# Optimization experiments

Measured on AMD Instinct MI355X. Metric: run time of the kernel, lower is better.

Reference implementation:

```python
import jax, jax.numpy as jnp
import numpy as np

NUM_HEADS = 12
D = 768
HD = D // NUM_HEADS  # 64

def setup_inputs() -> dict:
    key = jax.random.key(0)
    ks = jax.random.split(key, 9)
    s = 0.02
    return {
        "x": jax.random.normal(ks[0], (4, 2048, D), dtype=jnp.float32),
        "QW_w": jax.random.normal(ks[1], (D, D), dtype=jnp.float32) * s,
        "QW_b": jax.random.normal(ks[2], (D,), dtype=jnp.float32) * s,
        "KW_w": jax.random.normal(ks[3], (D, D), dtype=jnp.float32) * s,
        "KW_b": jax.random.normal(ks[4], (D,), dtype=jnp.float32) * s,
        "VW_w": jax.random.normal(ks[5], (D, D), dtype=jnp.float32) * s,
        "VW_b": jax.random.normal(ks[6], (D,), dtype=jnp.float32) * s,
        "OW_w": jax.random.normal(ks[7], (D, D), dtype=jnp.float32) * s,
        "OW_b": jax.random.normal(ks[8], (D,), dtype=jnp.float32) * s,
    }

def reference(x, QW_w, QW_b, KW_w, KW_b, VW_w, VW_b, OW_w, OW_b):
    b, s, _ = x.shape
    # torch nn.Linear: y = x @ W.T + b
    def proj(w, bias):
        y = jnp.einsum('bsd,ed->bse', x, w) + bias
        return y.reshape(b, s, NUM_HEADS, HD).transpose(0, 2, 1, 3)  # [b,h,s,hd]
    q = proj(QW_w, QW_b)
    k = proj(KW_w, KW_b)
    v = proj(VW_w, VW_b)
    scores = jnp.einsum('bhqd,bhkd->bhqk', q, k) / jnp.sqrt(jnp.float32(HD))
    attn = jax.nn.softmax(scores, axis=-1)
    out = jnp.einsum('bhqk,bhkd->bhqd', attn, v)
    out = out.transpose(0, 2, 1, 3).reshape(b, s, NUM_HEADS * HD)
    return jnp.einsum('bsd,ed->bse', out, OW_w) + OW_b
```

## Files before the change

kernel.cpp:

```cpp
#include <hip/hip_runtime.h>
#include <hip/hip_bf16.h>

#define NH  12
#define HD  64
#define DIM 768
#define SEQ 2048
#define NB  4
#define MM  (NB*SEQ)

typedef short v8s  __attribute__((ext_vector_type(8)));
typedef float v4f  __attribute__((ext_vector_type(4)));
typedef float v16f __attribute__((ext_vector_type(16)));

static __device__ __forceinline__ unsigned short f2b(float f) {
    unsigned int u = __float_as_uint(f);
    return (unsigned short)((u + 0x7FFFu + ((u >> 16) & 1u)) >> 16);
}
static __device__ __forceinline__ unsigned short f2b_fast(float f) {
    return (unsigned short)((__float_as_uint(f) + 0x8000u) >> 16);
}
static __device__ __forceinline__ void g2l16(const unsigned short* g, unsigned short* l) {
    __builtin_amdgcn_global_load_lds(
        (const __attribute__((address_space(1))) void*)g,
        (__attribute__((address_space(3))) void*)l, 16, 0, 0);
}

__global__ void cast_f32_bf16(const float* __restrict__ in,
                              unsigned short* __restrict__ out, int n4) {
    int i = blockIdx.x * blockDim.x + threadIdx.x;
    if (i < n4) {
        float4 v = reinterpret_cast<const float4*>(in)[i];
        ushort4 o;
        o.x = f2b(v.x); o.y = f2b(v.y); o.z = f2b(v.z); o.w = f2b(v.w);
        reinterpret_cast<ushort4*>(out)[i] = o;
    }
}

__global__ void cast4_f32_bf16(const float* __restrict__ i0, const float* __restrict__ i1,
                               const float* __restrict__ i2, const float* __restrict__ i3,
                               unsigned short* __restrict__ o0, unsigned short* __restrict__ o1,
                               unsigned short* __restrict__ o2, unsigned short* __restrict__ o3,
                               int n4) {
    int i = blockIdx.x * blockDim.x + threadIdx.x;
    if (i >= n4) return;
    const float* in; unsigned short* out;
    switch (blockIdx.y) {
        case 0: in = i0; out = o0; break;
        case 1: in = i1; out = o1; break;
        case 2: in = i2; out = o2; break;
        default: in = i3; out = o3; break;
    }
    float4 v = reinterpret_cast<const float4*>(in)[i];
    ushort4 o;
    o.x = f2b(v.x); o.y = f2b(v.y); o.z = f2b(v.z); o.w = f2b(v.w);
    reinterpret_cast<ushort4*>(out)[i] = o;
}

static __device__ __forceinline__ void gemm_core_128(
    const unsigned short* __restrict__ A,
    const unsigned short* __restrict__ W,
    int m0, int n0l,
    unsigned short* As, unsigned short* Bs,
    v4f acc[4][4])
{
    const int tid  = threadIdx.x;
    const int w    = tid >> 6, lane = tid & 63;
    const int quad = lane >> 4, l16 = lane & 15;
    const int wm   = w & 1,  wn = w >> 1;
    const int lane8 = lane >> 3, sc = lane & 7;

    #pragma unroll
    for (int i = 0; i < 4; ++i)
        #pragma unroll
        for (int j = 0; j < 4; ++j)
            acc[i][j] = v4f{0.f, 0.f, 0.f, 0.f};

    for (int kb = 0; kb < DIM; kb += 64) {
        __syncthreads();
        #pragma unroll
        for (int t = 0; t < 4; ++t) {
            int r8 = w * 32 + t * 8;
            int r  = r8 + lane8;
            int gch = sc ^ (r & 7);
            g2l16(&A[(size_t)(m0  + r) * DIM + kb + gch * 8], &As[r8 * 64]);
            g2l16(&W[(size_t)(n0l + r) * DIM + kb + gch * 8], &Bs[r8 * 64]);
        }
        __syncthreads();
        #pragma unroll
        for (int kk = 0; kk < 64; kk += 32) {
            v8s a[4], b[4];
            int chb = kk >> 3;
            #pragma unroll
            for (int i = 0; i < 4; ++i) {
                int m = wm * 64 + i * 16 + l16;
                a[i] = *reinterpret_cast<const v8s*>(
                    &As[m * 64 + (((chb + quad) ^ (m & 7)) << 3)]);
                int n = wn * 64 + i * 16 + l16;
                b[i] = *reinterpret_cast<const v8s*>(
                    &Bs[n * 64 + (((chb + quad) ^ (n & 7)) << 3)]);
            }
            #pragma unroll
            for (int i = 0; i < 4; ++i)
                #pragma unroll
                for (int j = 0; j < 4; ++j)
                    acc[i][j] = __builtin_amdgcn_mfma_f32_16x16x32_bf16(a[i], b[j], acc[i][j], 0, 0, 0);
        }
    }
}

__global__ __launch_bounds__(256) void gemm_qkv(
    const unsigned short* __restrict__ A,
    const unsigned short* __restrict__ Wq,
    const unsigned short* __restrict__ Wk,
    const unsigned short* __restrict__ Wv,
    const float* __restrict__ bq,
    const float* __restrict__ bk,
    const float* __restrict__ bvp,
    unsigned short* __restrict__ Qb,
    unsigned short* __restrict__ Kb,
    unsigned short* __restrict__ Vtb)
{
    __shared__ __align__(16) unsigned short As[128 * 64];
    __shared__ __align__(16) unsigned short Bs[128 * 64];

    const int m0   = blockIdx.x * 128;
    const int by   = blockIdx.y;
    const int wsel = by / 6;
    const int n0l  = (by % 6) * 128;
    const unsigned short* W    = (wsel == 0) ? Wq : (wsel == 1) ? Wk : Wv;
    const float*          bias = (wsel == 0) ? bq : (wsel == 1) ? bk : bvp;
    unsigned short*       out  = (wsel == 0) ? Qb : (wsel == 1) ? Kb : Vtb;
    const float scale = (wsel == 0) ? 0.1803368801f : 1.0f;

    v4f acc[4][4];
    gemm_core_128(A, W, m0, n0l, As, Bs, acc);

    const int tid  = threadIdx.x;
    const int w    = tid >> 6, lane = tid & 63;
    const int quad = lane >> 4, l16 = lane & 15;
    const int wm   = w & 1,  wn = w >> 1;

    #pragma unroll
    for (int i = 0; i < 4; ++i) {
        #pragma unroll
        for (int j = 0; j < 4; ++j) {
            int gnl = n0l + wn * 64 + j * 16 + l16;
            float bias_v = bias[gnl];
            int h = gnl >> 6, hd = gnl & 63;
            if (wsel == 2) {
                int gm0 = m0 + wm * 64 + i * 16 + quad * 4;
                int bb = gm0 >> 11, s0 = gm0 & (SEQ - 1);
                ushort4 pk;
                pk.x = f2b(acc[i][j][0] + bias_v);
                pk.y = f2b(acc[i][j][1] + bias_v);
                pk.z = f2b(acc[i][j][2] + bias_v);
                pk.w = f2b(acc[i][j][3] + bias_v);
                *reinterpret_cast<ushort4*>(
                    &out[((size_t)(bb * NH + h) * HD + hd) * SEQ + s0]) = pk;
            } else {
                #pragma unroll
                for (int r = 0; r < 4; ++r) {
                    int gm = m0 + wm * 64 + i * 16 + quad * 4 + r;
                    int bb = gm >> 11, s = gm & (SEQ - 1);
                    out[((size_t)(bb * NH + h) * SEQ + s) * HD + hd] =
                        f2b((acc[i][j][r] + bias_v) * scale);
                }
            }
        }
    }
}

__global__ __launch_bounds__(256) void gemm_o(
    const unsigned short* __restrict__ A,
    const unsigned short* __restrict__ W,
    const float* __restrict__ bias,
    float* __restrict__ out)
{
    __shared__ __align__(16) unsigned short As[128 * 64];
    __shared__ __align__(16) unsigned short Bs[128 * 64];

    const int m0  = blockIdx.x * 128;
    const int n0l = blockIdx.y * 128;

    v4f acc[4][4];
    gemm_core_128(A, W, m0, n0l, As, Bs, acc);

    const int tid  = threadIdx.x;
    const int w    = tid >> 6, lane = tid & 63;
    const int quad = lane >> 4, l16 = lane & 15;
    const int wm   = w & 1,  wn = w >> 1;

    #pragma unroll
    for (int i = 0; i < 4; ++i) {
        #pragma unroll
        for (int j = 0; j < 4; ++j) {
            int gn = n0l + wn * 64 + j * 16 + l16;
            float bias_v = bias[gn];
            #pragma unroll
            for (int r = 0; r < 4; ++r) {
                int gm = m0 + wm * 64 + i * 16 + quad * 4 + r;
                out[(size_t)gm * DIM + gn] = acc[i][j][r] + bias_v;
            }
        }
    }
}

__global__ __launch_bounds__(256, 3) void attn(
    const unsigned short* __restrict__ Q,
    const unsigned short* __restrict__ K,
    const unsigned short* __restrict__ Vt,
    unsigned short* __restrict__ ctx)
{
    __shared__ __align__(16) unsigned short Ks[2][64 * 64];
    __shared__ __align__(16) unsigned short Vs[2][64 * 64];
    __shared__ __align__(16) unsigned short Pl[4][32 * 64];

    const int tid  = threadIdx.x;
    const int w    = tid >> 6, lane = tid & 63;
    const int l31  = lane & 31, half = lane >> 5;
    const int lane8 = lane >> 3, sc = lane & 7;
    const int bh   = blockIdx.y;
    const int b    = bh / NH, h = bh % NH;
    const int q0   = blockIdx.x * 128 + w * 32;

    const unsigned short* Qp = Q  + ((size_t)bh * SEQ + q0) * HD;
    const unsigned short* Kp = K  + (size_t)bh * SEQ * HD;
    const unsigned short* Vp = Vt + (size_t)bh * HD * SEQ;
    unsigned short* Plw = &Pl[w][0];

    v8s aq[4];
    #pragma unroll
    for (int c = 0; c < 4; ++c)
        aq[c] = *reinterpret_cast<const v8s*>(&Qp[l31 * HD + c * 16 + half * 8]);

    v16f o0, o1;
    #pragma unroll
    for (int i = 0; i < 16; ++i) { o0[i] = 0.f; o1[i] = 0.f; }
    float li[16];
    #pragma unroll
    for (int i = 0; i < 16; ++i) li[i] = 0.f;

    const int rx = l31 & 7;
    int rdoff[4];
    #pragma unroll
    for (int c = 0; c < 4; ++c)
        rdoff[c] = l31 * 64 + (((c * 2 + half) ^ rx) << 3);

    const int c3 = l31 >> 3;
    int pwb[2][4];
    #pragma unroll
    for (int rr = 0; rr < 4; ++rr) {
        int base = rr * 64 + 256 * half + ((c3 ^ rr) << 3) + sc;
        pwb[0][rr] = base + 32 * half;
        pwb[1][rr] = base + 32 * (1 - half);
    }

    #define STAGE(kb_, buf_)                                                          \
        do {                                                                          \
            _Pragma("unroll")                                                         \
            for (int t = 0; t < 2; ++t) {                                             \
                int sb   = (t * 4 + w) * 64;                                          \
                int srow = (sb >> 3) + lane8;                                         \
                int gch  = sc ^ (srow & 7);                                           \
                g2l16(&Kp[(size_t)((kb_) + srow) * HD + gch * 8], &Ks[buf_][sb * 8]); \
                g2l16(&Vp[(size_t)srow * SEQ + (kb_) + gch * 8], &Vs[buf_][sb * 8]);  \
            }                                                                         \
        } while (0)

    STAGE(0, 0);

    #pragma unroll 2
    for (int it = 0; it < SEQ / 64; ++it) {
        const int buf = it & 1;
        __syncthreads();
        if (it + 1 < SEQ / 64) STAGE((it + 1) * 64, buf ^ 1);

        const unsigned short* Kb_ = &Ks[buf][0];
        const unsigned short* Vb_ = &Vs[buf][0];

        v16f s0, s1;
        #pragma unroll
        for (int i = 0; i < 16; ++i) { s0[i] = 0.f; s1[i] = 0.f; }
        #pragma unroll
        for (int c = 0; c < 4; ++c) {
            v8s k0 = *reinterpret_cast<const v8s*>(&Kb_[rdoff[c]]);
            v8s k1 = *reinterpret_cast<const v8s*>(&Kb_[rdoff[c] + 2048]);
            s0 = __builtin_amdgcn_mfma_f32_32x32x16_bf16(aq[c], k0, s0, 0, 0, 0);
            s1 = __builtin_amdgcn_mfma_f32_32x32x16_bf16(aq[c], k1, s1, 0, 0, 0);
        }

        #pragma unroll
        for (int reg = 0; reg < 16; ++reg) {
            float e0 = __builtin_exp2f(s0[reg]);
            float e1 = __builtin_exp2f(s1[reg]);
            li[reg] += e0 + e1;
            Plw[pwb[0][reg & 3] + (reg >> 2) * 512] = f2b_fast(e0);
            Plw[pwb[1][reg & 3] + (reg >> 2) * 512] = f2b_fast(e1);
        }

        #pragma unroll
        for (int c = 0; c < 4; ++c) {
            v8s pa = *reinterpret_cast<const v8s*>(&Plw[rdoff[c]]);
            v8s v0 = *reinterpret_cast<const v8s*>(&Vb_[rdoff[c]]);
            v8s v1 = *reinterpret_cast<const v8s*>(&Vb_[rdoff[c] + 2048]);
            o0 = __builtin_amdgcn_mfma_f32_32x32x16_bf16(pa, v0, o0, 0, 0, 0);
            o1 = __builtin_amdgcn_mfma_f32_32x32x16_bf16(pa, v1, o1, 0, 0, 0);
        }
    }
    #undef STAGE

    #pragma unroll
    for (int reg = 0; reg < 16; ++reg) {
        float t = li[reg];
        t += __shfl_xor(t, 1);
        t += __shfl_xor(t, 2);
        t += __shfl_xor(t, 4);
        t += __shfl_xor(t, 8);
        t += __shfl_xor(t, 16);
        float inv = 1.0f / t;
        int row = (reg & 3) + 8 * (reg >> 2) + 4 * half;
        int s = q0 + row;
        size_t base = ((size_t)(b * SEQ + s)) * DIM + h * HD;
        ctx[base + l31]      = f2b_fast(o0[reg] * inv);
        ctx[base + 32 + l31] = f2b_fast(o1[reg] * inv);
    }
}

extern "C" void kernel_launch(void* const* d_in, const int* in_sizes, int n_in,
                              void* d_out, int out_size, void* d_ws, size_t ws_size,
                              hipStream_t stream) {
    const float* x  = (const float*)d_in[0];
    const float* qw = (const float*)d_in[1]; const float* qb = (const float*)d_in[2];
    const float* kw = (const float*)d_in[3]; const float* kb = (const float*)d_in[4];
    const float* vw = (const float*)d_in[5]; const float* vb = (const float*)d_in[6];
    const float* ow = (const float*)d_in[7]; const float* ob = (const float*)d_in[8];
    float* out = (float*)d_out;

    char* ws = (char*)d_ws;
    size_t off = 0;
    auto alloc = [&](size_t bytes) -> unsigned short* {
        unsigned short* p = (unsigned short*)(ws + off);
        off += (bytes + 255) & ~(size_t)255;
        return p;
    };
    const size_t XB = (size_t)MM * DIM * 2;
    const size_t WB = (size_t)DIM * DIM * 2;
    const size_t QB = (size_t)NB * NH * SEQ * HD * 2;

    unsigned short* xb  = alloc(XB);
    unsigned short* wqb = alloc(WB);
    unsigned short* wkb = alloc(WB);
    unsigned short* wvb = alloc(WB);
    unsigned short* wob = alloc(WB);
    unsigned short* Qb  = alloc(QB);
    unsigned short* Kb  = alloc(QB);
    unsigned short* Vtb = alloc(QB);
    unsigned short* ctx = alloc(XB);

    const int n4x = MM * DIM / 4;
    const int n4w = DIM * DIM / 4;
    cast_f32_bf16<<<(n4x + 255) / 256, 256, 0, stream>>>(x, xb, n4x);
    cast4_f32_bf16<<<dim3((n4w + 255) / 256, 4), 256, 0, stream>>>(
        qw, kw, vw, ow, wqb, wkb, wvb, wob, n4w);

    gemm_qkv<<<dim3(MM / 128, 18), 256, 0, stream>>>(
        xb, wqb, wkb, wvb, qb, kb, vb, Qb, Kb, Vtb);

    attn<<<dim3(SEQ / 128, NB * NH), 256, 0, stream>>>(Qb, Kb, Vtb, ctx);

    gemm_o<<<dim3(MM / 128, DIM / 128), 256, 0, stream>>>(ctx, wob, ob, out);
}
```

Measured before the change: 249.8 us.

## Compute transposed attention scores so P stays in registers, load V directly

The attention kernel now computes S^T (K as the A operand, Q as B), so each lane holds scores for one query column. The exp'd probabilities are packed to bf16 pairs and exchanged across wave halves with shuffles instead of round-tripping through LDS. V is read straight from global memory into registers, with a prefetch for the next block, instead of being staged in shared memory. The row-sum becomes a single scalar per lane. This removes the P and V LDS traffic and cuts LDS footprint, at the cost of more registers, cross-lane shuffles and uncached-by-LDS global V loads.

```diff
diff --git a/kernel.cpp b/kernel.cpp
--- a/kernel.cpp
+++ b/kernel.cpp
@@ -8,16 +8,24 @@
 #define NB  4
 #define MM  (NB*SEQ)
 
-typedef short v8s  __attribute__((ext_vector_type(8)));
-typedef float v4f  __attribute__((ext_vector_type(4)));
-typedef float v16f __attribute__((ext_vector_type(16)));
+typedef short    v8s  __attribute__((ext_vector_type(8)));
+typedef float    v4f  __attribute__((ext_vector_type(4)));
+typedef float    v16f __attribute__((ext_vector_type(16)));
+typedef unsigned v4u  __attribute__((ext_vector_type(4)));
+
+#if __has_builtin(__builtin_amdgcn_exp2f)
+#define EXP2(x) __builtin_amdgcn_exp2f(x)
+#else
+#define EXP2(x) __builtin_exp2f(x)
+#endif
 
 static __device__ __forceinline__ unsigned short f2b(float f) {
     unsigned int u = __float_as_uint(f);
     return (unsigned short)((u + 0x7FFFu + ((u >> 16) & 1u)) >> 16);
 }
-static __device__ __forceinline__ unsigned short f2b_fast(float f) {
-    return (unsigned short)((__float_as_uint(f) + 0x8000u) >> 16);
+static __device__ __forceinline__ unsigned pk2bf(float lo, float hi) {
+    return __builtin_amdgcn_perm(__float_as_uint(hi) + 0x8000u,
+                                 __float_as_uint(lo) + 0x8000u, 0x07060302u);
 }
 static __device__ __forceinline__ void g2l16(const unsigned short* g, unsigned short* l) {
     __builtin_amdgcn_global_load_lds(
@@ -150,13 +158,13 @@
             if (wsel == 2) {
                 int gm0 = m0 + wm * 64 + i * 16 + quad * 4;
                 int bb = gm0 >> 11, s0 = gm0 & (SEQ - 1);
-                ushort4 pk;
-                pk.x = f2b(acc[i][j][0] + bias_v);
-                pk.y = f2b(acc[i][j][1] + bias_v);
-                pk.z = f2b(acc[i][j][2] + bias_v);
-                pk.w = f2b(acc[i][j][3] + bias_v);
+                ushort4 pkv;
+                pkv.x = f2b(acc[i][j][0] + bias_v);
+                pkv.y = f2b(acc[i][j][1] + bias_v);
+                pkv.z = f2b(acc[i][j][2] + bias_v);
+                pkv.w = f2b(acc[i][j][3] + bias_v);
                 *reinterpret_cast<ushort4*>(
-                    &out[((size_t)(bb * NH + h) * HD + hd) * SEQ + s0]) = pk;
+                    &out[((size_t)(bb * NH + h) * HD + hd) * SEQ + s0]) = pkv;
             } else {
                 #pragma unroll
                 for (int r = 0; r < 4; ++r) {
@@ -212,8 +220,6 @@
     unsigned short* __restrict__ ctx)
 {
     __shared__ __align__(16) unsigned short Ks[2][64 * 64];
-    __shared__ __align__(16) unsigned short Vs[2][64 * 64];
-    __shared__ __align__(16) unsigned short Pl[4][32 * 64];
 
     const int tid  = threadIdx.x;
     const int w    = tid >> 6, lane = tid & 63;
@@ -226,19 +232,24 @@
     const unsigned short* Qp = Q  + ((size_t)bh * SEQ + q0) * HD;
     const unsigned short* Kp = K  + (size_t)bh * SEQ * HD;
     const unsigned short* Vp = Vt + (size_t)bh * HD * SEQ;
-    unsigned short* Plw = &Pl[w][0];
-
-    v8s aq[4];
+
+    v8s bq[4];
     #pragma unroll
     for (int c = 0; c < 4; ++c)
-        aq[c] = *reinterpret_cast<const v8s*>(&Qp[l31 * HD + c * 16 + half * 8]);
-
-    v16f o0, o1;
-    #pragma unroll
-    for (int i = 0; i < 16; ++i) { o0[i] = 0.f; o1[i] = 0.f; }
-    float li[16];
-    #pragma unroll
-    for (int i = 0; i < 16; ++i) li[i] = 0.f;
+        bq[c] = *reinterpret_cast<const v8s*>(&Qp[l31 * HD + c * 16 + half * 8]);
+
+    v8s va[2][4];
+    #pragma unroll
+    for (int hb = 0; hb < 2; ++hb)
+        #pragma unroll
+        for (int c = 0; c < 4; ++c)
+            va[hb][c] = *reinterpret_cast<const v8s*>(
+                &Vp[(size_t)(hb * 32 + l31) * SEQ + c * 16 + half * 8]);
+
+    v16f o0, o1, Z;
+    #pragma unroll
+    for (int i = 0; i < 16; ++i) { o0[i] = 0.f; o1[i] = 0.f; Z[i] = 0.f; }
+    float li = 0.f;
 
     const int rx = l31 & 7;
     int rdoff[4];
@@ -246,83 +257,96 @@
     for (int c = 0; c < 4; ++c)
         rdoff[c] = l31 * 64 + (((c * 2 + half) ^ rx) << 3);
 
-    const int c3 = l31 >> 3;
-    int pwb[2][4];
-    #pragma unroll
-    for (int rr = 0; rr < 4; ++rr) {
-        int base = rr * 64 + 256 * half + ((c3 ^ rr) << 3) + sc;
-        pwb[0][rr] = base + 32 * half;
-        pwb[1][rr] = base + 32 * (1 - half);
-    }
-
-    #define STAGE(kb_, buf_)                                                          \
-        do {                                                                          \
-            _Pragma("unroll")                                                         \
-            for (int t = 0; t < 2; ++t) {                                             \
-                int sb   = (t * 4 + w) * 64;                                          \
-                int srow = (sb >> 3) + lane8;                                         \
-                int gch  = sc ^ (srow & 7);                                           \
-                g2l16(&Kp[(size_t)((kb_) + srow) * HD + gch * 8], &Ks[buf_][sb * 8]); \
-                g2l16(&Vp[(size_t)srow * SEQ + (kb_) + gch * 8], &Vs[buf_][sb * 8]);  \
-            }                                                                         \
+    #define STAGE_K(kb_, buf_)                                                       \
+        do {                                                                         \
+            _Pragma("unroll")                                                        \
+            for (int t = 0; t < 2; ++t) {                                            \
+                int r8  = (t * 4 + w) * 8;                                           \
+                int row = r8 + lane8;                                                \
+                int gch = sc ^ (row & 7);                                            \
+                g2l16(&Kp[(size_t)((kb_) + row) * HD + gch * 8], &Ks[buf_][r8 * 64]);\
+            }                                                                        \
         } while (0)
 
-    STAGE(0, 0);
-
-    #pragma unroll 2
+    STAGE_K(0, 0);
+
     for (int it = 0; it < SEQ / 64; ++it) {
         const int buf = it & 1;
+        const int kb  = it * 64;
         __syncthreads();
-        if (it + 1 < SEQ / 64) STAGE((it + 1) * 64, buf ^ 1);
-
-        const unsigned short* Kb_ = &Ks[buf][0];
-        const unsigned short* Vb_ = &Vs[buf][0];
-
-        v16f s0, s1;
-        #pragma unroll
-        for (int i = 0; i < 16; ++i) { s0[i] = 0.f; s1[i] = 0.f; }
-        #pragma unroll
-        for (int c = 0; c < 4; ++c) {
-            v8s k0 = *reinterpret_cast<const v8s*>(&Kb_[rdoff[c]]);
-            v8s k1 = *reinterpret_cast<const v8s*>(&Kb_[rdoff[c] + 2048]);
-            s0 = __builtin_amdgcn_mfma_f32_32x32x16_bf16(aq[c], k0, s0, 0, 0, 0);
-            s1 = __builtin_amdgcn_mfma_f32_32x32x16_bf16(aq[c], k1, s1, 0, 0, 0);
-        }
-
-        #pragma unroll
-        for (int reg = 0; reg < 16; ++reg) {
-            float e0 = __builtin_exp2f(s0[reg]);
-            float e1 = __builtin_exp2f(s1[reg]);
-            li[reg] += e0 + e1;
-            Plw[pwb[0][reg & 3] + (reg >> 2) * 512] = f2b_fast(e0);
-            Plw[pwb[1][reg & 3] + (reg >> 2) * 512] = f2b_fast(e1);
-        }
-
-        #pragma unroll
-        for (int c = 0; c < 4; ++c) {
-            v8s pa = *reinterpret_cast<const v8s*>(&Plw[rdoff[c]]);
-            v8s v0 = *reinterpret_cast<const v8s*>(&Vb_[rdoff[c]]);
-            v8s v1 = *reinterpret_cast<const v8s*>(&Vb_[rdoff[c] + 2048]);
-            o0 = __builtin_amdgcn_mfma_f32_32x32x16_bf16(pa, v0, o0, 0, 0, 0);
-            o1 = __builtin_amdgcn_mfma_f32_32x32x16_bf16(pa, v1, o1, 0, 0, 0);
-        }
-    }
-    #undef STAGE
-
-    #pragma unroll
-    for (int reg = 0; reg < 16; ++reg) {
-        float t = li[reg];
-        t += __shfl_xor(t, 1);
-        t += __shfl_xor(t, 2);
-        t += __shfl_xor(t, 4);
-        t += __shfl_xor(t, 8);
-        t += __shfl_xor(t, 16);
-        float inv = 1.0f / t;
-        int row = (reg & 3) + 8 * (reg >> 2) + 4 * half;
-        int s = q0 + row;
-        size_t base = ((size_t)(b * SEQ + s)) * DIM + h * HD;
-        ctx[base + l31]      = f2b_fast(o0[reg] * inv);
-        ctx[base + 32 + l31] = f2b_fast(o1[reg] * inv);
+        if (it + 1 < SEQ / 64) STAGE_K(kb + 64, buf ^ 1);
+
+        v16f s0 = Z, s1 = Z;
+        {
+            v8s ka00 = *reinterpret_cast<const v8s*>(&Ks[buf][rdoff[0]]);
+            v8s ka10 = *reinterpret_cast<const v8s*>(&Ks[buf][rdoff[0] + 2048]);
+            s0 = __builtin_amdgcn_mfma_f32_32x32x16_bf16(ka00, bq[0], Z, 0, 0, 0);
+            s1 = __builtin_amdgcn_mfma_f32_32x32x16_bf16(ka10, bq[0], Z, 0, 0, 0);
+            #pragma unroll
+            for (int c = 1; c < 4; ++c) {
+                v8s k0 = *reinterpret_cast<const v8s*>(&Ks[buf][rdoff[c]]);
+                v8s k1 = *reinterpret_cast<const v8s*>(&Ks[buf][rdoff[c] + 2048]);
+                s0 = __builtin_amdgcn_mfma_f32_32x32x16_bf16(k0, bq[c], s0, 0, 0, 0);
+                s1 = __builtin_amdgcn_mfma_f32_32x32x16_bf16(k1, bq[c], s1, 0, 0, 0);
+            }
+        }
+
+        unsigned pk[8][2];
+        #pragma unroll
+        for (int g = 0; g < 4; ++g) {
+            float e0 = EXP2(s0[4*g+0]), e1 = EXP2(s0[4*g+1]);
+            float e2 = EXP2(s0[4*g+2]), e3 = EXP2(s0[4*g+3]);
+            li += (e0 + e1) + (e2 + e3);
+            pk[g][0] = pk2bf(e0, e1);
+            pk[g][1] = pk2bf(e2, e3);
+            float f0 = EXP2(s1[4*g+0]), f1 = EXP2(s1[4*g+1]);
+            float f2 = EXP2(s1[4*g+2]), f3 = EXP2(s1[4*g+3]);
+            li += (f0 + f1) + (f2 + f3);
+            pk[4+g][0] = pk2bf(f0, f1);
+            pk[4+g][1] = pk2bf(f2, f3);
+        }
+
+        #pragma unroll
+        for (int cp = 0; cp < 4; ++cp) {
+            unsigned a0 = pk[2*cp][0],   a1 = pk[2*cp][1];
+            unsigned b0 = pk[2*cp+1][0], b1 = pk[2*cp+1][1];
+            unsigned xa0 = __shfl_xor(a0, 32), xa1 = __shfl_xor(a1, 32);
+            unsigned xb0 = __shfl_xor(b0, 32), xb1 = __shfl_xor(b1, 32);
+            v4u fw;
+            fw.x = half ? xb0 : a0;
+            fw.y = half ? xb1 : a1;
+            fw.z = half ? b0  : xa0;
+            fw.w = half ? b1  : xa1;
+            v8s pf = __builtin_bit_cast(v8s, fw);
+            o0 = __builtin_amdgcn_mfma_f32_32x32x16_bf16(va[0][cp], pf, o0, 0, 0, 0);
+            o1 = __builtin_amdgcn_mfma_f32_32x32x16_bf16(va[1][cp], pf, o1, 0, 0, 0);
+        }
+
+        if (it + 1 < SEQ / 64) {
+            #pragma unroll
+            for (int hb = 0; hb < 2; ++hb)
+                #pragma unroll
+                for (int c = 0; c < 4; ++c)
+                    va[hb][c] = *reinterpret_cast<const v8s*>(
+                        &Vp[(size_t)(hb * 32 + l31) * SEQ + kb + 64 + c * 16 + half * 8]);
+        }
+    }
+    #undef STAGE_K
+
+    float inv = 1.0f / (li + __shfl_xor(li, 32));
+
+    const int q = q0 + l31;
+    size_t base = ((size_t)(b * SEQ + q)) * DIM + h * HD;
+    #pragma unroll
+    for (int g = 0; g < 4; ++g) {
+        int hd0 = 8 * g + 4 * half;
+        uint2 u0, u1;
+        u0.x = pk2bf(o0[4*g+0] * inv, o0[4*g+1] * inv);
+        u0.y = pk2bf(o0[4*g+2] * inv, o0[4*g+3] * inv);
+        u1.x = pk2bf(o1[4*g+0] * inv, o1[4*g+1] * inv);
+        u1.y = pk2bf(o1[4*g+2] * inv, o1[4*g+3] * inv);
+        *reinterpret_cast<uint2*>(&ctx[base + hd0])      = u0;
+        *reinterpret_cast<uint2*>(&ctx[base + 32 + hd0]) = u1;
     }
 }
 
```

Measured after the change: 271.8 us. 1.09x slower.
